# Optimization experiments

Hardware: AMD Instinct MI355X
Metric: run time of the kernel (lower is better)

The kernel has to match this reference:

```python
import jax, jax.numpy as jnp
import numpy as np

ALPHA = 0.2  # LeakyReLU negative slope
NEG_INF = -9e15


def setup_inputs() -> dict:
    key = jax.random.key(0)
    k1, k2, k3, k4 = jax.random.split(key, 4)
    N, IN_F, OUT_F = 8192, 512, 256
    h = jax.random.normal(k1, (N, IN_F), dtype=jnp.float32)
    adj = jax.random.randint(k2, (N, N), 0, 2).astype(jnp.float32)
    # xavier_uniform for torch Linear weights
    limW = float(np.sqrt(6.0 / (IN_F + OUT_F)))
    W = jax.random.uniform(k3, (OUT_F, IN_F), dtype=jnp.float32, minval=-limW, maxval=limW)
    lima = float(np.sqrt(6.0 / (2 * OUT_F + 1)))
    a_vec = jax.random.uniform(k4, (2 * OUT_F,), dtype=jnp.float32, minval=-lima, maxval=lima)
    return {"h": h, "adj": adj, "W": W, "a_vec": a_vec}


def reference(h, adj, W, a_vec):
    # Wh = W(h), torch Linear: h @ W.T  -> [N, out]
    Wh = h @ W.T
    F_out = W.shape[0]
    # e_ij = leakyrelu(a . [Wh_i, Wh_j]) = leakyrelu(a1.Wh_i + a2.Wh_j)
    s_src = Wh @ a_vec[:F_out]   # [N] contribution of row i
    s_dst = Wh @ a_vec[F_out:]   # [N] contribution of col j
    e = jax.nn.leaky_relu(s_src[:, None] + s_dst[None, :], negative_slope=ALPHA)  # [N, N]
    scores = jnp.where(adj > 0, e, jnp.float32(NEG_INF))
    attention = jax.nn.softmax(scores, axis=1)
    # dropout is identity in eval mode
    h_prime = attention @ Wh  # [N, out]
    return h_prime, attention
```

## Files before the change

kernel.cpp:

```cpp
#include <hip/hip_runtime.h>
#include <stdint.h>

#define N_NODES 8192
#define IN_F    512
#define OUT_F   256
#define ALPHA   0.2f

typedef __attribute__((ext_vector_type(8))) short bf16x8;
typedef __attribute__((ext_vector_type(4))) float f32x4;

__device__ __forceinline__ uint32_t f32_to_bf16(float f) {
    union { float f; uint32_t u; } v; v.f = f;
    uint32_t u = v.u;
    return (u + 0x7fffu + ((u >> 16) & 1u)) >> 16;
}

__global__ __launch_bounds__(128) void k1_gemm_wh(
    const float* __restrict__ h, const float* __restrict__ W,
    const float* __restrict__ a_vec, float* __restrict__ wh,
    float* __restrict__ s_src, float* __restrict__ s_dst)
{
    const int cb = blockIdx.x;
    const int rb = blockIdx.y;
    const int i0 = rb * 128, n0 = cb * 64;
    const int t  = threadIdx.x;
    const int tm = t >> 3, tn = t & 7;

    __shared__ float As[32][132];
    __shared__ float Bs[32][68];

    float acc[8][8];
    #pragma unroll
    for (int i = 0; i < 8; i++)
        #pragma unroll
        for (int j = 0; j < 8; j++) acc[i][j] = 0.f;

    for (int k0 = 0; k0 < IN_F; k0 += 32) {
        __syncthreads();
        #pragma unroll
        for (int q = 0; q < 8; q++) {
            int u = q * 128 + t;
            int row = u >> 3;
            int ks  = (u & 7) * 4;
            float4 v = *(const float4*)&h[(size_t)(i0 + row) * IN_F + k0 + ks];
            As[ks + 0][row] = v.x; As[ks + 1][row] = v.y;
            As[ks + 2][row] = v.z; As[ks + 3][row] = v.w;
        }
        #pragma unroll
        for (int q = 0; q < 4; q++) {
            int u = q * 128 + t;
            int row = u >> 3;
            int ks  = (u & 7) * 4;
            float4 v = *(const float4*)&W[(size_t)(n0 + row) * IN_F + k0 + ks];
            Bs[ks + 0][row] = v.x; Bs[ks + 1][row] = v.y;
            Bs[ks + 2][row] = v.z; Bs[ks + 3][row] = v.w;
        }
        __syncthreads();
        #pragma unroll
        for (int kk = 0; kk < 32; kk++) {
            float a[8], b[8];
            *(float4*)&a[0] = *(const float4*)&As[kk][tm * 8];
            *(float4*)&a[4] = *(const float4*)&As[kk][tm * 8 + 4];
            *(float4*)&b[0] = *(const float4*)&Bs[kk][tn * 8];
            *(float4*)&b[4] = *(const float4*)&Bs[kk][tn * 8 + 4];
            #pragma unroll
            for (int i = 0; i < 8; i++)
                #pragma unroll
                for (int j = 0; j < 8; j++) acc[i][j] = fmaf(a[i], b[j], acc[i][j]);
        }
    }

    float a1[8], a2[8];
    #pragma unroll
    for (int j = 0; j < 8; j++) {
        a1[j] = a_vec[n0 + tn * 8 + j];
        a2[j] = a_vec[OUT_F + n0 + tn * 8 + j];
    }
    #pragma unroll
    for (int i = 0; i < 8; i++) {
        int gr = i0 + tm * 8 + i;
        *(float4*)&wh[(size_t)gr * OUT_F + n0 + tn * 8]     = *(float4*)&acc[i][0];
        *(float4*)&wh[(size_t)gr * OUT_F + n0 + tn * 8 + 4] = *(float4*)&acc[i][4];
        float v1 = 0.f, v2 = 0.f;
        #pragma unroll
        for (int j = 0; j < 8; j++) { v1 = fmaf(acc[i][j], a1[j], v1); v2 = fmaf(acc[i][j], a2[j], v2); }
        v1 += __shfl_xor(v1, 4, 64); v2 += __shfl_xor(v2, 4, 64);
        v1 += __shfl_xor(v1, 2, 64); v2 += __shfl_xor(v2, 2, 64);
        v1 += __shfl_xor(v1, 1, 64); v2 += __shfl_xor(v2, 1, 64);
        if (tn == 0) { atomicAdd(&s_src[gr], v1); atomicAdd(&s_dst[gr], v2); }
    }
}

__global__ __launch_bounds__(256) void k1c_whf(
    const float* __restrict__ wh, uint16_t* __restrict__ whf)
{
    const int c    = blockIdx.x * 4 + (threadIdx.x >> 6);
    const int lane = threadIdx.x & 63;
    const int ks   = c >> 4, nt = c & 15;
    const int rb   = ks * 32 + (lane >> 4) * 8;
    const int col  = nt * 16 + (lane & 15);
    uint32_t v[8];
    #pragma unroll
    for (int jj = 0; jj < 8; jj++)
        v[jj] = f32_to_bf16(wh[(size_t)(rb + jj) * OUT_F + col]);
    uint4 pk;
    pk.x = v[0] | (v[1] << 16);
    pk.y = v[2] | (v[3] << 16);
    pk.z = v[4] | (v[5] << 16);
    pk.w = v[6] | (v[7] << 16);
    *(uint4*)(whf + (size_t)c * 512 + lane * 8) = pk;
}

__global__ __launch_bounds__(256) void k2_mask_l(
    const float* __restrict__ adj, const float* __restrict__ s_src,
    const float* __restrict__ s_dst, uint64_t* __restrict__ mask,
    float* __restrict__ l_out)
{
    const int i = blockIdx.x;
    const int t = threadIdx.x;
    const int w = t >> 6, lane = t & 63;
    const float si = s_src[i];
    const float* row = adj + (size_t)i * N_NODES;
    float acc = 0.f;
    #pragma unroll 4
    for (int it = 0; it < 32; it++) {
        int j = it * 256 + t;
        float a = row[j];
        uint64_t m = __ballot(a > 0.f);
        if (lane == 0) mask[(size_t)i * 128 + it * 4 + w] = m;
        float x = si + s_dst[j];
        float e = fmaxf(x, ALPHA * x);
        float p = __expf(e);
        acc += (a > 0.f) ? p : 0.f;
    }
    #pragma unroll
    for (int off = 32; off >= 1; off >>= 1) acc += __shfl_xor(acc, off, 64);
    __shared__ float red[4];
    if (lane == 0) red[w] = acc;
    __syncthreads();
    if (t == 0) l_out[i] = (red[0] + red[1]) + (red[2] + red[3]);
}

__global__ __launch_bounds__(256) void k3_att_gemm(
    const uint64_t* __restrict__ mask, const float* __restrict__ s_src,
    const float* __restrict__ s_dst, const float* __restrict__ l_in,
    const uint16_t* __restrict__ whf, float* __restrict__ att_out,
    float* __restrict__ partial)
{
    const int rb = blockIdx.x, jc = blockIdx.y;
    const int i0 = rb * 64;
    const int jbase = jc * 2048;
    const int t = threadIdx.x;
    const int w = t >> 6, lane = t & 63;

    __shared__ uint16_t whf_lds[32 * 512];
    __shared__ uint16_t attf_lds[8 * 512];
    __shared__ uint64_t mw[2][64];
    __shared__ float    sd[2][64];
    __shared__ float    ssrc[64], invl[64];

    if (t < 64) {
        ssrc[t] = s_src[i0 + t];
        invl[t] = 1.0f / l_in[i0 + t];
        mw[0][t] = mask[(size_t)(i0 + t) * 128 + (jbase >> 6)];
        sd[0][t] = s_dst[jbase + t];
    }

    f32x4 acc[2][8];
    #pragma unroll
    for (int a = 0; a < 2; a++)
        #pragma unroll
        for (int b = 0; b < 8; b++) acc[a][b] = (f32x4){0.f, 0.f, 0.f, 0.f};

    const int mh = w & 1;
    const int nh = w >> 1;

    int cur = 0;
    for (int it = 0; it < 32; it++) {
        const int j0 = jbase + it * 64;
        __syncthreads();

        const uint16_t* src = whf + (size_t)(j0 >> 5) * 8192;
        #pragma unroll
        for (int q = 0; q < 8; q++) {
            int u = q * 256 + t;
            *(uint4*)(whf_lds + u * 8) = *(const uint4*)(src + u * 8);
        }

        #pragma unroll
        for (int q = 0; q < 2; q++) {
            int s    = q * 256 + t;
            int ks   = s >> 8;
            int mt   = (s >> 6) & 3;
            int ln   = s & 63;
            int m    = mt * 16 + (ln & 15);
            int kofs = ks * 32 + (ln >> 4) * 8;
            uint64_t mwv = mw[cur][m];
            float sim = ssrc[m], il = invl[m];
            float p[8];
            #pragma unroll
            for (int jj = 0; jj < 8; jj++) {
                float x  = sim + sd[cur][kofs + jj];
                float e  = fmaxf(x, ALPHA * x);
                float pe = __expf(e) * il;
                p[jj] = ((mwv >> (kofs + jj)) & 1ull) ? pe : 0.f;
            }
            float* go = att_out + (size_t)(i0 + m) * N_NODES + j0 + kofs;
            *(float4*)go       = *(float4*)&p[0];
            *(float4*)(go + 4) = *(float4*)&p[4];
            uint4 pk;
            pk.x = f32_to_bf16(p[0]) | (f32_to_bf16(p[1]) << 16);
            pk.y = f32_to_bf16(p[2]) | (f32_to_bf16(p[3]) << 16);
            pk.z = f32_to_bf16(p[4]) | (f32_to_bf16(p[5]) << 16);
            pk.w = f32_to_bf16(p[6]) | (f32_to_bf16(p[7]) << 16);
            *(uint4*)(attf_lds + (size_t)(ks * 4 + mt) * 512 + ln * 8) = pk;
        }

        if (it < 31 && t < 64) {
            int jn = j0 + 64;
            mw[cur ^ 1][t] = mask[(size_t)(i0 + t) * 128 + (jn >> 6)];
            sd[cur ^ 1][t] = s_dst[jn + t];
        }
        __syncthreads();

        #pragma unroll
        for (int ks = 0; ks < 2; ks++) {
            bf16x8 af[2];
            #pragma unroll
            for (int mi = 0; mi < 2; mi++) {
                int mt = mh * 2 + mi;
                af[mi] = *(const bf16x8*)(attf_lds + (size_t)(ks * 4 + mt) * 512 + lane * 8);
            }
            #pragma unroll
            for (int nl = 0; nl < 8; nl++) {
                int nt = nh * 8 + nl;
                bf16x8 bfr = *(const bf16x8*)(whf_lds + (size_t)(ks * 16 + nt) * 512 + lane * 8);
                acc[0][nl] = __builtin_amdgcn_mfma_f32_16x16x32_bf16(af[0], bfr, acc[0][nl], 0, 0, 0);
                acc[1][nl] = __builtin_amdgcn_mfma_f32_16x16x32_bf16(af[1], bfr, acc[1][nl], 0, 0, 0);
            }
        }
        cur ^= 1;
    }

    float* pbase = partial + (size_t)jc * ((size_t)N_NODES * OUT_F);
    #pragma unroll
    for (int mi = 0; mi < 2; mi++) {
        int gr0 = i0 + (mh * 2 + mi) * 16 + (lane >> 4) * 4;
        #pragma unroll
        for (int nl = 0; nl < 8; nl++) {
            int gc = nh * 128 + nl * 16 + (lane & 15);
            #pragma unroll
            for (int r = 0; r < 4; r++)
                pbase[(size_t)(gr0 + r) * OUT_F + gc] = acc[mi][nl][r];
        }
    }
}

__global__ __launch_bounds__(256) void k4_reduce(
    const float* __restrict__ partial, float* __restrict__ hp)
{
    const size_t S = (size_t)N_NODES * OUT_F;
    int idx = (blockIdx.x * 256 + threadIdx.x) * 4;
    float4 a = *(const float4*)(partial + idx);
    float4 b = *(const float4*)(partial + S + idx);
    float4 c = *(const float4*)(partial + 2 * S + idx);
    float4 d = *(const float4*)(partial + 3 * S + idx);
    float4 o;
    o.x = (a.x + b.x) + (c.x + d.x);
    o.y = (a.y + b.y) + (c.y + d.y);
    o.z = (a.z + b.z) + (c.z + d.z);
    o.w = (a.w + b.w) + (c.w + d.w);
    *(float4*)(hp + idx) = o;
}

extern "C" void kernel_launch(void* const* d_in, const int* in_sizes, int n_in,
                              void* d_out, int out_size, void* d_ws, size_t ws_size,
                              hipStream_t stream) {
    (void)in_sizes; (void)n_in; (void)out_size; (void)ws_size;
    const float* h     = (const float*)d_in[0];
    const float* adj   = (const float*)d_in[1];
    const float* W     = (const float*)d_in[2];
    const float* a_vec = (const float*)d_in[3];

    char* ws = (char*)d_ws;
    uint16_t* whf  = (uint16_t*)(ws);
    float* wh      = (float*)(ws + (size_t)(4u << 20));
    float* s_src   = (float*)(ws + (size_t)(12u << 20));
    float* s_dst   = (float*)(ws + (size_t)(12u << 20) + 32768);
    float* l_buf   = (float*)(ws + (size_t)(12u << 20) + 65536);
    uint64_t* mask = (uint64_t*)(ws + (size_t)(16u << 20));
    float* partial = (float*)(ws + (size_t)(24u << 20));

    float* hp  = (float*)d_out;
    float* att = hp + (size_t)N_NODES * OUT_F;

    hipMemsetAsync(s_src, 0, 65536, stream);
    k1_gemm_wh<<<dim3(4, 64), 128, 0, stream>>>(h, W, a_vec, wh, s_src, s_dst);
    k1c_whf<<<1024, 256, 0, stream>>>(wh, whf);
    k2_mask_l<<<8192, 256, 0, stream>>>(adj, s_src, s_dst, mask, l_buf);
    k3_att_gemm<<<dim3(128, 4), 256, 0, stream>>>(mask, s_src, s_dst, l_buf, whf, att, partial);
    k4_reduce<<<2048, 256, 0, stream>>>(partial, hp);
}
```

Before: 708.7 us.

## Restructure GAT pipeline: precompute score vectors, fuse Wh packing, retile attention GEMM

Computes the source and destination score vectors algebraically as h·(W^T a) through two new small kernels, so the Wh GEMM no longer needs atomics. The GEMM now writes bf16 MFMA-packed fragments directly, which removes the separate fp32 Wh buffer and the conversion kernel. The mask and row-sum kernel switches to float4 loads of adj. The attention kernel uses 32-row tiles (twice as many blocks), keeps attention fragments in registers instead of LDS, loads Wh with async global-to-LDS copies, and writes attention with nontemporal stores. The trade-offs are more kernel launches, scattered 2-byte stores in the pack step, and Wh tiles re-read by twice as many blocks.

Measured after the change: 640.4 us. -9.6%, faster.

```diff
diff --git a/kernel.cpp b/kernel.cpp
--- a/kernel.cpp
+++ b/kernel.cpp
@@ -15,100 +15,118 @@
     return (u + 0x7fffu + ((u >> 16) & 1u)) >> 16;
 }
 
-__global__ __launch_bounds__(128) void k1_gemm_wh(
+__device__ __forceinline__ void async_copy16(const void* g, void* l) {
+    __builtin_amdgcn_global_load_lds(
+        (const __attribute__((address_space(1))) uint32_t*)g,
+        (__attribute__((address_space(3))) uint32_t*)l, 16, 0, 0);
+}
+
+__global__ __launch_bounds__(256) void k0_wvec(
+    const float* __restrict__ W, const float* __restrict__ a_vec,
+    float* __restrict__ w12)
+{
+    const int t  = threadIdx.x;
+    const int nb = blockIdx.x * 8;
+    float a1lo = 0.f, a1hi = 0.f, a2lo = 0.f, a2hi = 0.f;
+    #pragma unroll
+    for (int q = 0; q < 8; q++) {
+        int n = nb + q;
+        float lo = W[(size_t)n * IN_F + t];
+        float hi = W[(size_t)n * IN_F + t + 256];
+        float a1 = a_vec[n], a2 = a_vec[OUT_F + n];
+        a1lo = fmaf(lo, a1, a1lo); a1hi = fmaf(hi, a1, a1hi);
+        a2lo = fmaf(lo, a2, a2lo); a2hi = fmaf(hi, a2, a2hi);
+    }
+    atomicAdd(&w12[t], a1lo);       atomicAdd(&w12[t + 256], a1hi);
+    atomicAdd(&w12[512 + t], a2lo); atomicAdd(&w12[512 + t + 256], a2hi);
+}
+
+__global__ __launch_bounds__(256) void ks_svec(
+    const float* __restrict__ h, const float* __restrict__ w12,
+    float* __restrict__ s_src, float* __restrict__ s_dst)
+{
+    __shared__ float sw[1024];
+    const int t = threadIdx.x;
+    #pragma unroll
+    for (int q = 0; q < 4; q++) sw[q * 256 + t] = w12[q * 256 + t];
+    __syncthreads();
+    const int w = t >> 6, ln = t & 63;
+    const int i = blockIdx.x * 4 + w;
+    const float* hr = h + (size_t)i * IN_F + ln * 8;
+    float4 h0 = *(const float4*)hr;
+    float4 h1 = *(const float4*)(hr + 4);
+    const float* w1 = sw + ln * 8;
+    const float* w2 = sw + 512 + ln * 8;
+    float v1 = h0.x*w1[0] + h0.y*w1[1] + h0.z*w1[2] + h0.w*w1[3]
+             + h1.x*w1[4] + h1.y*w1[5] + h1.z*w1[6] + h1.w*w1[7];
+    float v2 = h0.x*w2[0] + h0.y*w2[1] + h0.z*w2[2] + h0.w*w2[3]
+             + h1.x*w2[4] + h1.y*w2[5] + h1.z*w2[6] + h1.w*w2[7];
+    #pragma unroll
+    for (int off = 32; off >= 1; off >>= 1) {
+        v1 += __shfl_xor(v1, off, 64);
+        v2 += __shfl_xor(v2, off, 64);
+    }
+    if (ln == 0) { s_src[i] = v1; s_dst[i] = v2; }
+}
+
+__global__ __launch_bounds__(256) void k1_wh_pack(
     const float* __restrict__ h, const float* __restrict__ W,
-    const float* __restrict__ a_vec, float* __restrict__ wh,
-    float* __restrict__ s_src, float* __restrict__ s_dst)
-{
-    const int cb = blockIdx.x;
-    const int rb = blockIdx.y;
-    const int i0 = rb * 128, n0 = cb * 64;
+    uint16_t* __restrict__ whf)
+{
+    const int n0 = blockIdx.x * 64, i0 = blockIdx.y * 64;
     const int t  = threadIdx.x;
-    const int tm = t >> 3, tn = t & 7;
-
-    __shared__ float As[32][132];
-    __shared__ float Bs[32][68];
-
-    float acc[8][8];
-    #pragma unroll
-    for (int i = 0; i < 8; i++)
-        #pragma unroll
-        for (int j = 0; j < 8; j++) acc[i][j] = 0.f;
+    const int tn = t & 15, tm = t >> 4;
+
+    __shared__ float As[32][65];
+    __shared__ float Bs[32][65];
+
+    float acc[4][4];
+    #pragma unroll
+    for (int i = 0; i < 4; i++)
+        #pragma unroll
+        for (int j = 0; j < 4; j++) acc[i][j] = 0.f;
 
     for (int k0 = 0; k0 < IN_F; k0 += 32) {
         __syncthreads();
         #pragma unroll
-        for (int q = 0; q < 8; q++) {
-            int u = q * 128 + t;
+        for (int q = 0; q < 2; q++) {
+            int u   = q * 256 + t;
             int row = u >> 3;
-            int ks  = (u & 7) * 4;
-            float4 v = *(const float4*)&h[(size_t)(i0 + row) * IN_F + k0 + ks];
-            As[ks + 0][row] = v.x; As[ks + 1][row] = v.y;
-            As[ks + 2][row] = v.z; As[ks + 3][row] = v.w;
-        }
-        #pragma unroll
-        for (int q = 0; q < 4; q++) {
-            int u = q * 128 + t;
-            int row = u >> 3;
-            int ks  = (u & 7) * 4;
-            float4 v = *(const float4*)&W[(size_t)(n0 + row) * IN_F + k0 + ks];
-            Bs[ks + 0][row] = v.x; Bs[ks + 1][row] = v.y;
-            Bs[ks + 2][row] = v.z; Bs[ks + 3][row] = v.w;
+            int kf  = (u & 7) * 4;
+            float4 va = *(const float4*)&h[(size_t)(i0 + row) * IN_F + k0 + kf];
+            As[kf + 0][row] = va.x; As[kf + 1][row] = va.y;
+            As[kf + 2][row] = va.z; As[kf + 3][row] = va.w;
+            float4 vb = *(const float4*)&W[(size_t)(n0 + row) * IN_F + k0 + kf];
+            Bs[kf + 0][row] = vb.x; Bs[kf + 1][row] = vb.y;
+            Bs[kf + 2][row] = vb.z; Bs[kf + 3][row] = vb.w;
         }
         __syncthreads();
         #pragma unroll
         for (int kk = 0; kk < 32; kk++) {
-            float a[8], b[8];
-            *(float4*)&a[0] = *(const float4*)&As[kk][tm * 8];
-            *(float4*)&a[4] = *(const float4*)&As[kk][tm * 8 + 4];
-            *(float4*)&b[0] = *(const float4*)&Bs[kk][tn * 8];
-            *(float4*)&b[4] = *(const float4*)&Bs[kk][tn * 8 + 4];
+            float a[4], b[4];
+            *(float4*)a = *(const float4*)&As[kk][tm * 4];
+            *(float4*)b = *(const float4*)&Bs[kk][tn * 4];
             #pragma unroll
-            for (int i = 0; i < 8; i++)
+            for (int i = 0; i < 4; i++)
                 #pragma unroll
-                for (int j = 0; j < 8; j++) acc[i][j] = fmaf(a[i], b[j], acc[i][j]);
-        }
-    }
-
-    float a1[8], a2[8];
-    #pragma unroll
-    for (int j = 0; j < 8; j++) {
-        a1[j] = a_vec[n0 + tn * 8 + j];
-        a2[j] = a_vec[OUT_F + n0 + tn * 8 + j];
-    }
-    #pragma unroll
-    for (int i = 0; i < 8; i++) {
-        int gr = i0 + tm * 8 + i;
-        *(float4*)&wh[(size_t)gr * OUT_F + n0 + tn * 8]     = *(float4*)&acc[i][0];
-        *(float4*)&wh[(size_t)gr * OUT_F + n0 + tn * 8 + 4] = *(float4*)&acc[i][4];
-        float v1 = 0.f, v2 = 0.f;
-        #pragma unroll
-        for (int j = 0; j < 8; j++) { v1 = fmaf(acc[i][j], a1[j], v1); v2 = fmaf(acc[i][j], a2[j], v2); }
-        v1 += __shfl_xor(v1, 4, 64); v2 += __shfl_xor(v2, 4, 64);
-        v1 += __shfl_xor(v1, 2, 64); v2 += __shfl_xor(v2, 2, 64);
-        v1 += __shfl_xor(v1, 1, 64); v2 += __shfl_xor(v2, 1, 64);
-        if (tn == 0) { atomicAdd(&s_src[gr], v1); atomicAdd(&s_dst[gr], v2); }
-    }
-}
-
-__global__ __launch_bounds__(256) void k1c_whf(
-    const float* __restrict__ wh, uint16_t* __restrict__ whf)
-{
-    const int c    = blockIdx.x * 4 + (threadIdx.x >> 6);
-    const int lane = threadIdx.x & 63;
-    const int ks   = c >> 4, nt = c & 15;
-    const int rb   = ks * 32 + (lane >> 4) * 8;
-    const int col  = nt * 16 + (lane & 15);
-    uint32_t v[8];
-    #pragma unroll
-    for (int jj = 0; jj < 8; jj++)
-        v[jj] = f32_to_bf16(wh[(size_t)(rb + jj) * OUT_F + col]);
-    uint4 pk;
-    pk.x = v[0] | (v[1] << 16);
-    pk.y = v[2] | (v[3] << 16);
-    pk.z = v[4] | (v[5] << 16);
-    pk.w = v[6] | (v[7] << 16);
-    *(uint4*)(whf + (size_t)c * 512 + lane * 8) = pk;
+                for (int j = 0; j < 4; j++) acc[i][j] = fmaf(a[i], b[j], acc[i][j]);
+        }
+    }
+
+    #pragma unroll
+    for (int ii = 0; ii < 4; ii++) {
+        int gr = i0 + tm * 4 + ii;
+        int ck = gr >> 5;
+        int lr = (gr >> 3) & 3;
+        int jj = gr & 7;
+        #pragma unroll
+        for (int jn = 0; jn < 4; jn++) {
+            int gc   = n0 + tn * 4 + jn;
+            int c    = ck * 16 + (gc >> 4);
+            int lane = (gc & 15) + lr * 16;
+            whf[(size_t)c * 512 + lane * 8 + jj] = (uint16_t)f32_to_bf16(acc[ii][jn]);
+        }
+    }
 }
 
 __global__ __launch_bounds__(256) void k2_mask_l(
@@ -117,26 +135,35 @@
     float* __restrict__ l_out)
 {
     const int i = blockIdx.x;
-    const int t = threadIdx.x;
-    const int w = t >> 6, lane = t & 63;
+    const int t = threadIdx.x, w = t >> 6, ln = t & 63;
     const float si = s_src[i];
-    const float* row = adj + (size_t)i * N_NODES;
+    const float4* rowv = (const float4*)(adj + (size_t)i * N_NODES);
+    const float4* sdv  = (const float4*)s_dst;
     float acc = 0.f;
-    #pragma unroll 4
-    for (int it = 0; it < 32; it++) {
-        int j = it * 256 + t;
-        float a = row[j];
-        uint64_t m = __ballot(a > 0.f);
-        if (lane == 0) mask[(size_t)i * 128 + it * 4 + w] = m;
-        float x = si + s_dst[j];
-        float e = fmaxf(x, ALPHA * x);
-        float p = __expf(e);
-        acc += (a > 0.f) ? p : 0.f;
+    #pragma unroll 2
+    for (int it = 0; it < 8; it++) {
+        int jb = it * 4 + w;
+        int v4 = jb * 64 + ln;
+        float4 a  = rowv[v4];
+        float4 sd = sdv[v4];
+        uint64_t b0 = __ballot(a.x > 0.f);
+        uint64_t b1 = __ballot(a.y > 0.f);
+        uint64_t b2 = __ballot(a.z > 0.f);
+        uint64_t b3 = __ballot(a.w > 0.f);
+        if (ln == 0) {
+            uint64_t* mw = mask + (size_t)i * 128 + jb * 4;
+            mw[0] = b0; mw[1] = b1; mw[2] = b2; mw[3] = b3;
+        }
+        float x, e;
+        x = si + sd.x; e = fmaxf(x, ALPHA * x); if (a.x > 0.f) acc += __expf(e);
+        x = si + sd.y; e = fmaxf(x, ALPHA * x); if (a.y > 0.f) acc += __expf(e);
+        x = si + sd.z; e = fmaxf(x, ALPHA * x); if (a.z > 0.f) acc += __expf(e);
+        x = si + sd.w; e = fmaxf(x, ALPHA * x); if (a.w > 0.f) acc += __expf(e);
     }
     #pragma unroll
     for (int off = 32; off >= 1; off >>= 1) acc += __shfl_xor(acc, off, 64);
     __shared__ float red[4];
-    if (lane == 0) red[w] = acc;
+    if (ln == 0) red[w] = acc;
     __syncthreads();
     if (t == 0) l_out[i] = (red[0] + red[1]) + (red[2] + red[3]);
 }
@@ -148,32 +175,28 @@
     float* __restrict__ partial)
 {
     const int rb = blockIdx.x, jc = blockIdx.y;
-    const int i0 = rb * 64;
-    const int jbase = jc * 2048;
-    const int t = threadIdx.x;
-    const int w = t >> 6, lane = t & 63;
-
-    __shared__ uint16_t whf_lds[32 * 512];
-    __shared__ uint16_t attf_lds[8 * 512];
-    __shared__ uint64_t mw[2][64];
+    const int i0 = rb * 32, jbase = jc * 2048;
+    const int t = threadIdx.x, w = t >> 6, ln = t & 63;
+    const int mh = w & 1, nh = w >> 1;
+
+    __shared__ uint16_t whf_lds[16384];
+    __shared__ uint64_t mw[2][32][4];
     __shared__ float    sd[2][64];
-    __shared__ float    ssrc[64], invl[64];
-
-    if (t < 64) {
-        ssrc[t] = s_src[i0 + t];
-        invl[t] = 1.0f / l_in[i0 + t];
-        mw[0][t] = mask[(size_t)(i0 + t) * 128 + (jbase >> 6)];
-        sd[0][t] = s_dst[jbase + t];
-    }
-
-    f32x4 acc[2][8];
-    #pragma unroll
-    for (int a = 0; a < 2; a++)
-        #pragma unroll
-        for (int b = 0; b < 8; b++) acc[a][b] = (f32x4){0.f, 0.f, 0.f, 0.f};
-
-    const int mh = w & 1;
-    const int nh = w >> 1;
+    __shared__ float    ssrc[32], invl[32];
+
+    if (t < 32) { ssrc[t] = s_src[i0 + t]; invl[t] = 1.0f / l_in[i0 + t]; }
+    if (t < 64) sd[0][t] = s_dst[jbase + t];
+    if (t >= 64 && t < 192) {
+        int r = (t - 64) >> 2, ph = t & 3;
+        mw[0][r][ph] = mask[(size_t)(i0 + r) * 128 + (jbase >> 8) * 4 + ph];
+    }
+
+    f32x4 acc[8];
+    #pragma unroll
+    for (int b = 0; b < 8; b++) acc[b] = (f32x4){0.f, 0.f, 0.f, 0.f};
+
+    const int m   = mh * 16 + (ln & 15);
+    const int kof = (ln >> 4) * 8;
 
     int cur = 0;
     for (int it = 0; it < 32; it++) {
@@ -183,76 +206,76 @@
         const uint16_t* src = whf + (size_t)(j0 >> 5) * 8192;
         #pragma unroll
         for (int q = 0; q < 8; q++) {
-            int u = q * 256 + t;
-            *(uint4*)(whf_lds + u * 8) = *(const uint4*)(src + u * 8);
-        }
-
-        #pragma unroll
-        for (int q = 0; q < 2; q++) {
-            int s    = q * 256 + t;
-            int ks   = s >> 8;
-            int mt   = (s >> 6) & 3;
-            int ln   = s & 63;
-            int m    = mt * 16 + (ln & 15);
-            int kofs = ks * 32 + (ln >> 4) * 8;
-            uint64_t mwv = mw[cur][m];
-            float sim = ssrc[m], il = invl[m];
-            float p[8];
+            int c = w * 8 + q;
+            async_copy16(src + (size_t)c * 512 + ln * 8, whf_lds + c * 512);
+        }
+
+        uint64_t mwv[4];
+        #pragma unroll
+        for (int ph = 0; ph < 4; ph++) mwv[ph] = mw[cur][m][ph];
+        float sim = ssrc[m], il = invl[m];
+        int bbase = ((it & 3) << 4) + (kof >> 2);
+        float p[2][8];
+        #pragma unroll
+        for (int ks = 0; ks < 2; ks++) {
             #pragma unroll
             for (int jj = 0; jj < 8; jj++) {
-                float x  = sim + sd[cur][kofs + jj];
+                float x  = sim + sd[cur][ks * 32 + kof + jj];
                 float e  = fmaxf(x, ALPHA * x);
                 float pe = __expf(e) * il;
-                p[jj] = ((mwv >> (kofs + jj)) & 1ull) ? pe : 0.f;
+                int bidx = bbase + ks * 8 + (jj >> 2);
+                p[ks][jj] = ((mwv[jj & 3] >> bidx) & 1ull) ? pe : 0.f;
             }
-            float* go = att_out + (size_t)(i0 + m) * N_NODES + j0 + kofs;
-            *(float4*)go       = *(float4*)&p[0];
-            *(float4*)(go + 4) = *(float4*)&p[4];
-            uint4 pk;
-            pk.x = f32_to_bf16(p[0]) | (f32_to_bf16(p[1]) << 16);
-            pk.y = f32_to_bf16(p[2]) | (f32_to_bf16(p[3]) << 16);
-            pk.z = f32_to_bf16(p[4]) | (f32_to_bf16(p[5]) << 16);
-            pk.w = f32_to_bf16(p[6]) | (f32_to_bf16(p[7]) << 16);
-            *(uint4*)(attf_lds + (size_t)(ks * 4 + mt) * 512 + ln * 8) = pk;
-        }
-
-        if (it < 31 && t < 64) {
+        }
+
+        if (nh == 0) {
+            float* go = att_out + (size_t)(i0 + m) * N_NODES + j0 + kof;
+            __builtin_nontemporal_store(*(f32x4*)&p[0][0], (f32x4*)go);
+            __builtin_nontemporal_store(*(f32x4*)&p[0][4], (f32x4*)(go + 4));
+            __builtin_nontemporal_store(*(f32x4*)&p[1][0], (f32x4*)(go + 32));
+            __builtin_nontemporal_store(*(f32x4*)&p[1][4], (f32x4*)(go + 36));
+        }
+
+        bf16x8 af[2];
+        #pragma unroll
+        for (int ks = 0; ks < 2; ks++) {
+            union { bf16x8 v; uint32_t u[4]; } pk;
+            #pragma unroll
+            for (int q = 0; q < 4; q++)
+                pk.u[q] = f32_to_bf16(p[ks][2 * q]) | (f32_to_bf16(p[ks][2 * q + 1]) << 16);
+            af[ks] = pk.v;
+        }
+
+        if (it < 31) {
             int jn = j0 + 64;
-            mw[cur ^ 1][t] = mask[(size_t)(i0 + t) * 128 + (jn >> 6)];
-            sd[cur ^ 1][t] = s_dst[jn + t];
+            if (t < 64) sd[cur ^ 1][t] = s_dst[jn + t];
+            else if (t < 192) {
+                int r = (t - 64) >> 2, ph = t & 3;
+                mw[cur ^ 1][r][ph] = mask[(size_t)(i0 + r) * 128 + (jn >> 8) * 4 + ph];
+            }
         }
         __syncthreads();
 
         #pragma unroll
         for (int ks = 0; ks < 2; ks++) {
-            bf16x8 af[2];
-            #pragma unroll
-            for (int mi = 0; mi < 2; mi++) {
-                int mt = mh * 2 + mi;
-                af[mi] = *(const bf16x8*)(attf_lds + (size_t)(ks * 4 + mt) * 512 + lane * 8);
-            }
             #pragma unroll
             for (int nl = 0; nl < 8; nl++) {
                 int nt = nh * 8 + nl;
-                bf16x8 bfr = *(const bf16x8*)(whf_lds + (size_t)(ks * 16 + nt) * 512 + lane * 8);
-                acc[0][nl] = __builtin_amdgcn_mfma_f32_16x16x32_bf16(af[0], bfr, acc[0][nl], 0, 0, 0);
-                acc[1][nl] = __builtin_amdgcn_mfma_f32_16x16x32_bf16(af[1], bfr, acc[1][nl], 0, 0, 0);
+                bf16x8 bfr = *(const bf16x8*)(whf_lds + (size_t)(ks * 16 + nt) * 512 + ln * 8);
+                acc[nl] = __builtin_amdgcn_mfma_f32_16x16x32_bf16(af[ks], bfr, acc[nl], 0, 0, 0);
             }
         }
         cur ^= 1;
     }
 
     float* pbase = partial + (size_t)jc * ((size_t)N_NODES * OUT_F);
-    #pragma unroll
-    for (int mi = 0; mi < 2; mi++) {
-        int gr0 = i0 + (mh * 2 + mi) * 16 + (lane >> 4) * 4;
-        #pragma unroll
-        for (int nl = 0; nl < 8; nl++) {
-            int gc = nh * 128 + nl * 16 + (lane & 15);
-            #pragma unroll
-            for (int r = 0; r < 4; r++)
-                pbase[(size_t)(gr0 + r) * OUT_F + gc] = acc[mi][nl][r];
-        }
+    int gr0 = i0 + mh * 16 + (ln >> 4) * 4;
+    #pragma unroll
+    for (int nl = 0; nl < 8; nl++) {
+        int gc = nh * 128 + nl * 16 + (ln & 15);
+        #pragma unroll
+        for (int r = 0; r < 4; r++)
+            pbase[(size_t)(gr0 + r) * OUT_F + gc] = acc[nl][r];
     }
 }
 
@@ -284,20 +307,21 @@
 
     char* ws = (char*)d_ws;
     uint16_t* whf  = (uint16_t*)(ws);
-    float* wh      = (float*)(ws + (size_t)(4u << 20));
-    float* s_src   = (float*)(ws + (size_t)(12u << 20));
-    float* s_dst   = (float*)(ws + (size_t)(12u << 20) + 32768);
-    float* l_buf   = (float*)(ws + (size_t)(12u << 20) + 65536);
-    uint64_t* mask = (uint64_t*)(ws + (size_t)(16u << 20));
-    float* partial = (float*)(ws + (size_t)(24u << 20));
+    uint64_t* mask = (uint64_t*)(ws + ((size_t)4 << 20));
+    float* partial = (float*)(ws + ((size_t)12 << 20));
+    float* w12     = (float*)(ws + ((size_t)44 << 20));
+    float* s_src   = (float*)(ws + ((size_t)44 << 20) + 16384);
+    float* s_dst   = (float*)(ws + ((size_t)44 << 20) + 16384 + 32768);
+    float* l_buf   = (float*)(ws + ((size_t)44 << 20) + 16384 + 65536);
 
     float* hp  = (float*)d_out;
     float* att = hp + (size_t)N_NODES * OUT_F;
 
-    hipMemsetAsync(s_src, 0, 65536, stream);
-    k1_gemm_wh<<<dim3(4, 64), 128, 0, stream>>>(h, W, a_vec, wh, s_src, s_dst);
-    k1c_whf<<<1024, 256, 0, stream>>>(wh, whf);
+    hipMemsetAsync(w12, 0, 4096, stream);
+    k0_wvec<<<32, 256, 0, stream>>>(W, a_vec, w12);
+    ks_svec<<<2048, 256, 0, stream>>>(h, w12, s_src, s_dst);
+    k1_wh_pack<<<dim3(4, 128), 256, 0, stream>>>(h, W, whf);
     k2_mask_l<<<8192, 256, 0, stream>>>(adj, s_src, s_dst, mask, l_buf);
-    k3_att_gemm<<<dim3(128, 4), 256, 0, stream>>>(mask, s_src, s_dst, l_buf, whf, att, partial);
+    k3_att_gemm<<<dim3(256, 4), 256, 0, stream>>>(mask, s_src, s_dst, l_buf, whf, att, partial);
     k4_reduce<<<2048, 256, 0, stream>>>(partial, hp);
 }
```
